# Kernel optimization log

Hardware: AMD Instinct MI355X
Metric: run time of the kernel (lower is better)

The kernel has to match this reference:

```python
import jax, jax.numpy as jnp
import numpy as np

NUM_VARS = 64
LAG = 16
H1 = 64
H2 = 1024
NUM_OUT = 1
BATCH = 16384


def setup_inputs() -> dict:
    key = jax.random.key(0)
    ks = jax.random.split(key, 8)

    def xavier(k, shape, fan_in, fan_out):
        std = float(np.sqrt(2.0 / (fan_in + fan_out)))
        return jax.random.normal(k, shape, dtype=jnp.float32) * std

    inputs = jax.random.normal(ks[0], (BATCH, NUM_VARS * LAG), dtype=jnp.float32)
    # Per-variable sub-network weights, batched over the variable axis.
    W1 = xavier(ks[1], (NUM_VARS, LAG, H1), LAG, H1)
    b1 = jnp.full((NUM_VARS, H1), 0.1, dtype=jnp.float32)
    W2 = xavier(ks[2], (NUM_VARS, H1, H1), H1, H1)
    b2 = jnp.full((NUM_VARS, H1), 0.1, dtype=jnp.float32)
    imp = (jnp.ones((NUM_VARS,), dtype=jnp.float32) / NUM_VARS
           + 1e-5 * jax.random.normal(ks[3], (NUM_VARS,), dtype=jnp.float32))
    W3 = xavier(ks[4], (NUM_VARS * H1, H2), NUM_VARS * H1, H2)
    b3 = jnp.full((H2,), 0.1, dtype=jnp.float32)
    W4 = xavier(ks[5], (H2, NUM_OUT), H2, NUM_OUT)
    b4 = jnp.full((NUM_OUT,), 0.1, dtype=jnp.float32)
    return {"inputs": inputs, "W1": W1, "b1": b1, "W2": W2, "b2": b2,
            "imp": imp, "W3": W3, "b3": b3, "W4": W4, "b4": b4}


def reference(inputs, W1, b1, W2, b2, imp, W3, b3, W4, b4):
    B = inputs.shape[0]
    # [B, V*lag] -> [B, V, lag]; slicing inputs[:, lag*i:lag*(i+1)] == x[:, i, :]
    x = inputs.reshape(B, NUM_VARS, LAG)
    # dp = 0.0 -> dropout is identity
    h = jax.nn.relu(jnp.einsum('bvl,vlh->bvh', x, W1) + b1[None])      # [B, V, H1]
    h = jax.nn.relu(jnp.einsum('bvh,vhk->bvk', h, W2) + b2[None])      # [B, V, H1]
    agg = (h * imp[None, :, None]).reshape(B, NUM_VARS * H1)            # weighted concat
    pred = jax.nn.relu(agg @ W3 + b3) @ W4 + b4                        # [B, NUM_OUT]
    return pred
```

## Files before the change

### kernel.cpp

```cpp
#include <hip/hip_runtime.h>
#include <hip/hip_bf16.h>
#include <stdint.h>

#define B_ROWS 16384
#define NVARS 64
#define LAG 16
#define H1 64
#define H2 1024
#define KDIM (NVARS * H1)

typedef __attribute__((ext_vector_type(8))) short short8;
typedef __attribute__((ext_vector_type(4))) short short4v;
typedef __attribute__((ext_vector_type(4))) float f32x4;

typedef __attribute__((address_space(3))) uint8_t lds_u8;
typedef const __attribute__((address_space(1))) uint8_t glob_u8;

__device__ __forceinline__ void gload_lds16(const void* g, void* l) {
    __builtin_amdgcn_global_load_lds((glob_u8*)g, (lds_u8*)l, 16, 0, 0);
}

__device__ __forceinline__ short f2bf_s(float x) {
    __hip_bfloat16 h = __float2bfloat16(x);
    return *(short*)&h;
}
__device__ __forceinline__ float bf_s2f(short s) {
    __hip_bfloat16 h = *(__hip_bfloat16*)&s;
    return __bfloat162float(h);
}

__global__ __launch_bounds__(256) void misc_pre_kernel(
    const float* __restrict__ w3, const float* __restrict__ b4,
    const float* __restrict__ W1, const float* __restrict__ W2,
    __hip_bfloat16* __restrict__ w3t, float* __restrict__ out,
    short* __restrict__ w1bh, short* __restrict__ w1bl,
    short* __restrict__ w2bh, short* __restrict__ w2bl) {
    __shared__ float tile[64][65];
    const int bid = blockIdx.x;
    const int t = threadIdx.x;

    if (bid < 1024) {
        const int k0 = (bid >> 4) * 64;
        const int n0 = (bid & 15) * 64;
        const int c = t & 63, r0 = t >> 6;
#pragma unroll
        for (int i = 0; i < 16; i++) {
            int r = r0 + i * 4;
            tile[r][c] = w3[(size_t)(k0 + r) * H2 + n0 + c];
        }
        __syncthreads();
#pragma unroll
        for (int i = 0; i < 16; i++) {
            int nr = r0 + i * 4;
            w3t[(size_t)(n0 + nr) * KDIM + k0 + c] = __float2bfloat16(tile[c][nr]);
        }
        return;
    }
    if (bid < 1088) {
        out[(bid - 1024) * 256 + t] = b4[0];
        return;
    }

    const int v = bid - 1088;
    for (int idx = t; idx < 64 * 32; idx += 256) {
        int col = idx >> 5, k = idx & 31;
        float wv = W1[((size_t)v * LAG + (k & 15)) * H1 + col];
        short hi = f2bf_s(wv);
        w1bh[((size_t)v * 64 + col) * 40 + k] = hi;
        w1bl[((size_t)v * 64 + col) * 40 + k] = (k < 16) ? f2bf_s(wv - bf_s2f(hi)) : (short)0;
    }
    for (int idx = t; idx < 64 * 64; idx += 256) {
        int col = idx >> 6, k = idx & 63;
        float wv = W2[((size_t)v * H1 + k) * H1 + col];
        short hi = f2bf_s(wv);
        w2bh[((size_t)v * 64 + col) * 72 + k] = hi;
        w2bl[((size_t)v * 64 + col) * 72 + k] = f2bf_s(wv - bf_s2f(hi));
    }
}

__global__ __launch_bounds__(256) void subnets_mfma_kernel(
    const float* __restrict__ inputs, const float* __restrict__ b1g,
    const float* __restrict__ b2g, const float* __restrict__ impg,
    const short* __restrict__ w1bh_g, const short* __restrict__ w1bl_g,
    const short* __restrict__ w2bh_g, const short* __restrict__ w2bl_g,
    __hip_bfloat16* __restrict__ agg) {
    const int v = blockIdx.x >> 7;
    const int b0 = (blockIdx.x & 127) * 128;
    const int t = threadIdx.x;
    const int lane = t & 63, wv = t >> 6;
    const int l15 = lane & 15, g = lane >> 4;

    __shared__ __align__(16) char smem[38912];
    short* xsS   = (short*)smem;
    short* w1bhS = (short*)(smem + 10240);
    short* w1blS = (short*)(smem + 15360);
    short* Hs    = (short*)smem;
    short* w2bhS = (short*)(smem + 20480);
    short* w2blS = (short*)(smem + 29696);

    for (int c = t; c < 320; c += 256) {
        gload_lds16(w1bh_g + (size_t)v * 2560 + c * 8, (char*)w1bhS + c * 16);
        gload_lds16(w1bl_g + (size_t)v * 2560 + c * 8, (char*)w1blS + c * 16);
    }
    for (int c = t; c < 576; c += 256) {
        gload_lds16(w2bh_g + (size_t)v * 4608 + c * 8, (char*)w2bhS + c * 16);
        gload_lds16(w2bl_g + (size_t)v * 4608 + c * 8, (char*)w2blS + c * 16);
    }
#pragma unroll
    for (int i = 0; i < 2; i++) {
        int idx = t + i * 256;
        int row = idx >> 2, seg = idx & 3;
        float4 x4 = *(const float4*)(inputs + (size_t)(b0 + row) * (NVARS * LAG) + v * LAG + seg * 4);
        const float* xp = (const float*)&x4;
        short4v hv, lv;
#pragma unroll
        for (int j = 0; j < 4; j++) {
            short hi = f2bf_s(xp[j]);
            hv[j] = hi;
            lv[j] = f2bf_s(xp[j] - bf_s2f(hi));
        }
        *(short4v*)&xsS[row * 40 + seg * 4] = hv;
        *(short4v*)&xsS[row * 40 + 16 + seg * 4] = lv;
    }
    __syncthreads();

    short8 a1[2], b1hF[4], b1lF[4];
#pragma unroll
    for (int mt = 0; mt < 2; mt++)
        a1[mt] = *(const short8*)&xsS[(wv * 32 + mt * 16 + l15) * 40 + g * 8];
#pragma unroll
    for (int nt = 0; nt < 4; nt++) {
        b1hF[nt] = *(const short8*)&w1bhS[(nt * 16 + l15) * 40 + g * 8];
        b1lF[nt] = *(const short8*)&w1blS[(nt * 16 + l15) * 40 + g * 8];
    }
    f32x4 acc1[2][4];
#pragma unroll
    for (int mt = 0; mt < 2; mt++)
#pragma unroll
        for (int nt = 0; nt < 4; nt++) {
            acc1[mt][nt] = (f32x4){0.f, 0.f, 0.f, 0.f};
            acc1[mt][nt] = __builtin_amdgcn_mfma_f32_16x16x32_bf16(a1[mt], b1hF[nt], acc1[mt][nt], 0, 0, 0);
            acc1[mt][nt] = __builtin_amdgcn_mfma_f32_16x16x32_bf16(a1[mt], b1lF[nt], acc1[mt][nt], 0, 0, 0);
        }
    __syncthreads();

#pragma unroll
    for (int mt = 0; mt < 2; mt++)
#pragma unroll
        for (int nt = 0; nt < 4; nt++) {
            int col = nt * 16 + l15;
            float bias = b1g[v * H1 + col];
#pragma unroll
            for (int r = 0; r < 4; r++) {
                float h = fmaxf(acc1[mt][nt][r] + bias, 0.f);
                int row = wv * 32 + mt * 16 + g * 4 + r;
                Hs[row * 72 + col] = f2bf_s(h);
            }
        }
    __syncthreads();

    short8 a2[2][2], b2hF[4][2], b2lF[4][2];
#pragma unroll
    for (int mt = 0; mt < 2; mt++)
#pragma unroll
        for (int kc = 0; kc < 2; kc++)
            a2[mt][kc] = *(const short8*)&Hs[(wv * 32 + mt * 16 + l15) * 72 + kc * 32 + g * 8];
#pragma unroll
    for (int nt = 0; nt < 4; nt++)
#pragma unroll
        for (int kc = 0; kc < 2; kc++) {
            b2hF[nt][kc] = *(const short8*)&w2bhS[(nt * 16 + l15) * 72 + kc * 32 + g * 8];
            b2lF[nt][kc] = *(const short8*)&w2blS[(nt * 16 + l15) * 72 + kc * 32 + g * 8];
        }
    f32x4 acc2[2][4];
#pragma unroll
    for (int mt = 0; mt < 2; mt++)
#pragma unroll
        for (int nt = 0; nt < 4; nt++) {
            f32x4 a = (f32x4){0.f, 0.f, 0.f, 0.f};
            a = __builtin_amdgcn_mfma_f32_16x16x32_bf16(a2[mt][0], b2hF[nt][0], a, 0, 0, 0);
            a = __builtin_amdgcn_mfma_f32_16x16x32_bf16(a2[mt][1], b2hF[nt][1], a, 0, 0, 0);
            a = __builtin_amdgcn_mfma_f32_16x16x32_bf16(a2[mt][0], b2lF[nt][0], a, 0, 0, 0);
            a = __builtin_amdgcn_mfma_f32_16x16x32_bf16(a2[mt][1], b2lF[nt][1], a, 0, 0, 0);
            acc2[mt][nt] = a;
        }

    const float impv = impg[v];
#pragma unroll
    for (int mt = 0; mt < 2; mt++)
#pragma unroll
        for (int nt = 0; nt < 4; nt++) {
            int col = nt * 16 + l15;
            float bias = b2g[v * H1 + col];
#pragma unroll
            for (int r = 0; r < 4; r++) {
                float o = fmaxf(acc2[mt][nt][r] + bias, 0.f) * impv;
                int row = b0 + wv * 32 + mt * 16 + g * 4 + r;
                agg[(size_t)row * KDIM + v * H1 + col] = __float2bfloat16(o);
            }
        }
}

#define NT 128

__global__ __launch_bounds__(512, 2) void gemm3_kernel(
    const __hip_bfloat16* __restrict__ agg,
    const __hip_bfloat16* __restrict__ w3t,
    const float* __restrict__ b3, const float* __restrict__ W4,
    float* __restrict__ out) {
    const int bid = ((blockIdx.x & 7) << 5) + (blockIdx.x >> 3);
    const int brow = (bid >> 2) * 256;
    const int bcol = (bid & 3) * 256;
    const int t = threadIdx.x;
    const int lane = t & 63;
    const int wid = t >> 6;
    const int wm = wid >> 2, wn = wid & 3;
    const int l15 = lane & 15, g = lane >> 4;

    __shared__ __align__(16) char smem[131072];

    const int c0 = t, c1 = t + 512;
    const int r0 = c0 >> 2, r1 = c1 >> 2;
    const int col0 = ((c0 & 3) * 8) ^ ((r0 & 8) ? 16 : 0);
    const int col1 = ((c1 & 3) * 8) ^ ((r1 & 8) ? 16 : 0);
    const __hip_bfloat16* aS0 = agg + (size_t)(brow + r0) * KDIM + col0;
    const __hip_bfloat16* aS1 = agg + (size_t)(brow + r1) * KDIM + col1;
    const __hip_bfloat16* bS0 = w3t + (size_t)(bcol + r0) * KDIM + col0;
    const __hip_bfloat16* bS1 = w3t + (size_t)(bcol + r1) * KDIM + col1;

#define STAGE_A(p, kt) do { \
        gload_lds16(aS0 + (kt) * 32, smem + (p) * 32768 + c0 * 16); \
        gload_lds16(aS1 + (kt) * 32, smem + (p) * 32768 + c1 * 16); } while (0)
#define STAGE_B(p, kt) do { \
        gload_lds16(bS0 + (kt) * 32, smem + (p) * 32768 + 16384 + c0 * 16); \
        gload_lds16(bS1 + (kt) * 32, smem + (p) * 32768 + 16384 + c1 * 16); } while (0)

    const int coff = (g * 16) ^ ((l15 & 8) ? 32 : 0);
    const int aBase = (wm * 128 + l15) * 64 + coff;
    const int bBase = 16384 + (wn * 64 + l15) * 64 + coff;

#define LDA(i, p) fa[i] = *(const short8*)(smem + (p) * 32768 + aBase + (i) * 1024)
#define LDB(i, p) fb[i] = *(const short8*)(smem + (p) * 32768 + bBase + (i) * 1024)

    short8 fa[8], fb[4];
    f32x4 acc[8][4];
#pragma unroll
    for (int m = 0; m < 8; m++)
#pragma unroll
        for (int n = 0; n < 4; n++) acc[m][n] = (f32x4){0.f, 0.f, 0.f, 0.f};

    STAGE_A(0, 0); STAGE_B(0, 0);
    STAGE_A(1, 1); STAGE_B(1, 1);
    STAGE_A(2, 2); STAGE_B(2, 2);
    asm volatile("s_waitcnt vmcnt(8)" ::: "memory");
    __builtin_amdgcn_s_barrier();
    __builtin_amdgcn_sched_barrier(0);

#define PH_A(p, DOSTAGE, kt3) do { \
        LDA(0, p); LDA(1, p); LDA(2, p); LDA(3, p); \
        LDB(0, p); LDB(1, p); LDB(2, p); LDB(3, p); \
        if (DOSTAGE) STAGE_A((kt3) & 3, kt3); \
        __builtin_amdgcn_s_setprio(1); \
        _Pragma("unroll") \
        for (int mm = 0; mm < 4; mm++) \
            _Pragma("unroll") \
            for (int nn = 0; nn < 4; nn++) \
                acc[mm][nn] = __builtin_amdgcn_mfma_f32_16x16x32_bf16( \
                    fa[mm], fb[nn], acc[mm][nn], 0, 0, 0); \
        __builtin_amdgcn_s_setprio(0); } while (0)

#define PH_B(p, DOSTAGE, kt3, VMSTR) do { \
        LDA(4, p); LDA(5, p); LDA(6, p); LDA(7, p); \
        if (DOSTAGE) STAGE_B((kt3) & 3, kt3); \
        __builtin_amdgcn_s_setprio(1); \
        _Pragma("unroll") \
        for (int mm = 0; mm < 4; mm++) \
            _Pragma("unroll") \
            for (int nn = 0; nn < 4; nn++) \
                acc[4 + mm][nn] = __builtin_amdgcn_mfma_f32_16x16x32_bf16( \
                    fa[4 + mm], fb[nn], acc[4 + mm][nn], 0, 0, 0); \
        __builtin_amdgcn_s_setprio(0); \
        asm volatile(VMSTR ::: "memory"); \
        __builtin_amdgcn_s_barrier(); \
        __builtin_amdgcn_sched_barrier(0); } while (0)

#pragma unroll 4
    for (int tt = 0; tt < NT - 4; ++tt) {
        const int p = tt & 3;
        PH_A(p, 1, tt + 3);
        PH_B(p, 1, tt + 3, "s_waitcnt vmcnt(8)");
    }
    PH_A(0, 1, 127); PH_B(0, 1, 127, "s_waitcnt vmcnt(8)");
    PH_A(1, 0, 0);   PH_B(1, 0, 0, "s_waitcnt vmcnt(4)");
    PH_A(2, 0, 0);   PH_B(2, 0, 0, "s_waitcnt vmcnt(0)");
    PH_A(3, 0, 0);   PH_B(3, 0, 0, "s_waitcnt vmcnt(0)");

    float bias[4], w4v[4];
#pragma unroll
    for (int n = 0; n < 4; n++) {
        int col = bcol + wn * 64 + n * 16 + l15;
        bias[n] = b3[col];
        w4v[n] = W4[col];
    }
#pragma unroll
    for (int m = 0; m < 8; m++) {
        float pr0 = 0.f, pr1 = 0.f, pr2 = 0.f, pr3 = 0.f;
#pragma unroll
        for (int n = 0; n < 4; n++) {
            pr0 += fmaxf(acc[m][n][0] + bias[n], 0.f) * w4v[n];
            pr1 += fmaxf(acc[m][n][1] + bias[n], 0.f) * w4v[n];
            pr2 += fmaxf(acc[m][n][2] + bias[n], 0.f) * w4v[n];
            pr3 += fmaxf(acc[m][n][3] + bias[n], 0.f) * w4v[n];
        }
#pragma unroll
        for (int mask = 1; mask < 16; mask <<= 1) {
            pr0 += __shfl_xor(pr0, mask, 64);
            pr1 += __shfl_xor(pr1, mask, 64);
            pr2 += __shfl_xor(pr2, mask, 64);
            pr3 += __shfl_xor(pr3, mask, 64);
        }
        if (l15 == 0) {
            int row = brow + wm * 128 + m * 16 + g * 4;
            atomicAdd(&out[row + 0], pr0);
            atomicAdd(&out[row + 1], pr1);
            atomicAdd(&out[row + 2], pr2);
            atomicAdd(&out[row + 3], pr3);
        }
    }
}

extern "C" void kernel_launch(void* const* d_in, const int* in_sizes, int n_in,
                              void* d_out, int out_size, void* d_ws, size_t ws_size,
                              hipStream_t stream) {
    const float* inputs = (const float*)d_in[0];
    const float* W1 = (const float*)d_in[1];
    const float* b1 = (const float*)d_in[2];
    const float* W2 = (const float*)d_in[3];
    const float* b2 = (const float*)d_in[4];
    const float* imp = (const float*)d_in[5];
    const float* W3 = (const float*)d_in[6];
    const float* b3 = (const float*)d_in[7];
    const float* W4 = (const float*)d_in[8];
    const float* b4 = (const float*)d_in[9];
    float* out = (float*)d_out;

    char* ws = (char*)d_ws;
    const size_t agg_bytes = (size_t)B_ROWS * KDIM * 2;
    const size_t w3t_bytes = (size_t)H2 * KDIM * 2;
    const size_t w1b_bytes = (size_t)NVARS * 64 * 40 * 2;
    const size_t w2b_bytes = (size_t)NVARS * 64 * 72 * 2;

    __hip_bfloat16* agg = (__hip_bfloat16*)ws;
    __hip_bfloat16* w3t = (__hip_bfloat16*)(ws + agg_bytes);
    short* w1bh = (short*)(ws + agg_bytes + w3t_bytes);
    short* w1bl = (short*)(ws + agg_bytes + w3t_bytes + w1b_bytes);
    short* w2bh = (short*)(ws + agg_bytes + w3t_bytes + 2 * w1b_bytes);
    short* w2bl = (short*)(ws + agg_bytes + w3t_bytes + 2 * w1b_bytes + w2b_bytes);

    hipLaunchKernelGGL(misc_pre_kernel, dim3(1152), dim3(256), 0, stream,
                       W3, b4, W1, W2, w3t, out, w1bh, w1bl, w2bh, w2bl);
    hipLaunchKernelGGL(subnets_mfma_kernel, dim3(NVARS * (B_ROWS / 128)), dim3(256), 0, stream,
                       inputs, b1, b2, imp, w1bh, w1bl, w2bh, w2bl, agg);
    hipLaunchKernelGGL(gemm3_kernel, dim3((B_ROWS / 256) * (H2 / 256)), dim3(512), 0, stream,
                       agg, w3t, b3, W4, out);
}
```

Baseline: 167.2 us.

## Double-buffer MFMA fragments in registers and merge A/B staging per tile

The main GEMM loop now reads the next K-tile's LDS fragments into a second register set while MFMAs run on the current set. This ping-pongs between two fragment buffers instead of splitting each tile into two phases. The A and B global-to-LDS stage loads are merged into one issue per tile, and the vmcnt waits are adjusted to match. The aim is to hide LDS read latency behind MFMA work. In exchange, the second fragment set costs about 48 extra VGPRs on top of the 128 accumulator registers, which raises register pressure and the risk of spills.

Result: slower. 183.8 us (+9.9%).

```diff
diff --git a/kernel.cpp b/kernel.cpp
--- a/kernel.cpp
+++ b/kernel.cpp
@@ -228,10 +228,9 @@
     const __hip_bfloat16* bS0 = w3t + (size_t)(bcol + r0) * KDIM + col0;
     const __hip_bfloat16* bS1 = w3t + (size_t)(bcol + r1) * KDIM + col1;
 
-#define STAGE_A(p, kt) do { \
+#define STAGE_AB(p, kt) do { \
         gload_lds16(aS0 + (kt) * 32, smem + (p) * 32768 + c0 * 16); \
-        gload_lds16(aS1 + (kt) * 32, smem + (p) * 32768 + c1 * 16); } while (0)
-#define STAGE_B(p, kt) do { \
+        gload_lds16(aS1 + (kt) * 32, smem + (p) * 32768 + c1 * 16); \
         gload_lds16(bS0 + (kt) * 32, smem + (p) * 32768 + 16384 + c0 * 16); \
         gload_lds16(bS1 + (kt) * 32, smem + (p) * 32768 + 16384 + c1 * 16); } while (0)
 
@@ -239,61 +238,57 @@
     const int aBase = (wm * 128 + l15) * 64 + coff;
     const int bBase = 16384 + (wn * 64 + l15) * 64 + coff;
 
-#define LDA(i, p) fa[i] = *(const short8*)(smem + (p) * 32768 + aBase + (i) * 1024)
-#define LDB(i, p) fb[i] = *(const short8*)(smem + (p) * 32768 + bBase + (i) * 1024)
-
-    short8 fa[8], fb[4];
-    f32x4 acc[8][4];
-#pragma unroll
-    for (int m = 0; m < 8; m++)
-#pragma unroll
-        for (int n = 0; n < 4; n++) acc[m][n] = (f32x4){0.f, 0.f, 0.f, 0.f};
-
-    STAGE_A(0, 0); STAGE_B(0, 0);
-    STAGE_A(1, 1); STAGE_B(1, 1);
-    STAGE_A(2, 2); STAGE_B(2, 2);
-    asm volatile("s_waitcnt vmcnt(8)" ::: "memory");
-    __builtin_amdgcn_s_barrier();
-    __builtin_amdgcn_sched_barrier(0);
-
-#define PH_A(p, DOSTAGE, kt3) do { \
-        LDA(0, p); LDA(1, p); LDA(2, p); LDA(3, p); \
-        LDB(0, p); LDB(1, p); LDB(2, p); LDB(3, p); \
-        if (DOSTAGE) STAGE_A((kt3) & 3, kt3); \
+#define RD(p, off) (*(const short8*)(smem + (p) * 32768 + (off)))
+#define LDFRAGS(FA, FB, p) do { \
+        FA[0] = RD(p, aBase + 0 * 1024); FA[1] = RD(p, aBase + 1 * 1024); \
+        FA[2] = RD(p, aBase + 2 * 1024); FA[3] = RD(p, aBase + 3 * 1024); \
+        FA[4] = RD(p, aBase + 4 * 1024); FA[5] = RD(p, aBase + 5 * 1024); \
+        FA[6] = RD(p, aBase + 6 * 1024); FA[7] = RD(p, aBase + 7 * 1024); \
+        FB[0] = RD(p, bBase + 0 * 1024); FB[1] = RD(p, bBase + 1 * 1024); \
+        FB[2] = RD(p, bBase + 2 * 1024); FB[3] = RD(p, bBase + 3 * 1024); } while (0)
+
+#define MM(FA, FB) do { \
         __builtin_amdgcn_s_setprio(1); \
         _Pragma("unroll") \
-        for (int mm = 0; mm < 4; mm++) \
+        for (int mm = 0; mm < 8; mm++) \
             _Pragma("unroll") \
             for (int nn = 0; nn < 4; nn++) \
                 acc[mm][nn] = __builtin_amdgcn_mfma_f32_16x16x32_bf16( \
-                    fa[mm], fb[nn], acc[mm][nn], 0, 0, 0); \
+                    FA[mm], FB[nn], acc[mm][nn], 0, 0, 0); \
         __builtin_amdgcn_s_setprio(0); } while (0)
 
-#define PH_B(p, DOSTAGE, kt3, VMSTR) do { \
-        LDA(4, p); LDA(5, p); LDA(6, p); LDA(7, p); \
-        if (DOSTAGE) STAGE_B((kt3) & 3, kt3); \
-        __builtin_amdgcn_s_setprio(1); \
-        _Pragma("unroll") \
-        for (int mm = 0; mm < 4; mm++) \
-            _Pragma("unroll") \
-            for (int nn = 0; nn < 4; nn++) \
-                acc[4 + mm][nn] = __builtin_amdgcn_mfma_f32_16x16x32_bf16( \
-                    fa[4 + mm], fb[nn], acc[4 + mm][nn], 0, 0, 0); \
-        __builtin_amdgcn_s_setprio(0); \
+#define TILE(FAc, FBc, FAn, FBn, tn, DOPREF, DOSTAGE, kt3, VMSTR) do { \
+        if (DOPREF) LDFRAGS(FAn, FBn, (tn) & 3); \
+        if (DOSTAGE) STAGE_AB((kt3) & 3, kt3); \
+        MM(FAc, FBc); \
         asm volatile(VMSTR ::: "memory"); \
         __builtin_amdgcn_s_barrier(); \
         __builtin_amdgcn_sched_barrier(0); } while (0)
 
+    short8 fa0[8], fb0[4], fa1[8], fb1[4];
+    f32x4 acc[8][4];
+#pragma unroll
+    for (int m = 0; m < 8; m++)
+#pragma unroll
+        for (int n = 0; n < 4; n++) acc[m][n] = (f32x4){0.f, 0.f, 0.f, 0.f};
+
+    STAGE_AB(0, 0);
+    STAGE_AB(1, 1);
+    STAGE_AB(2, 2);
+    asm volatile("s_waitcnt vmcnt(4)" ::: "memory");
+    __builtin_amdgcn_s_barrier();
+    __builtin_amdgcn_sched_barrier(0);
+    LDFRAGS(fa0, fb0, 0);
+
 #pragma unroll 4
     for (int tt = 0; tt < NT - 4; ++tt) {
-        const int p = tt & 3;
-        PH_A(p, 1, tt + 3);
-        PH_B(p, 1, tt + 3, "s_waitcnt vmcnt(8)");
-    }
-    PH_A(0, 1, 127); PH_B(0, 1, 127, "s_waitcnt vmcnt(8)");
-    PH_A(1, 0, 0);   PH_B(1, 0, 0, "s_waitcnt vmcnt(4)");
-    PH_A(2, 0, 0);   PH_B(2, 0, 0, "s_waitcnt vmcnt(0)");
-    PH_A(3, 0, 0);   PH_B(3, 0, 0, "s_waitcnt vmcnt(0)");
+        if (tt & 1) TILE(fa1, fb1, fa0, fb0, tt + 1, 1, 1, tt + 3, "s_waitcnt vmcnt(4)");
+        else        TILE(fa0, fb0, fa1, fb1, tt + 1, 1, 1, tt + 3, "s_waitcnt vmcnt(4)");
+    }
+    TILE(fa0, fb0, fa1, fb1, 125, 1, 1, 127, "s_waitcnt vmcnt(4)");
+    TILE(fa1, fb1, fa0, fb0, 126, 1, 0, 0,   "s_waitcnt vmcnt(0)");
+    TILE(fa0, fb0, fa1, fb1, 127, 1, 0, 0,   "s_waitcnt vmcnt(0)");
+    MM(fa1, fb1);
 
     float bias[4], w4v[4];
 #pragma unroll
```
